# Kernel optimization log

Measured on AMD Instinct MI355X. Metric: run time of the kernel, lower is better.

The kernel has to match this reference:

```python
import jax, jax.numpy as jnp
import numpy as np

B, T, C, H = 4, 2048, 1024, 16
D = C // H  # head_dim = 64


def setup_inputs() -> dict:
    key = jax.random.key(0)
    ks = jax.random.split(key, 10)
    s = 1.0 / np.sqrt(C)
    inp = {
        "x": jax.random.normal(ks[0], (B, T, C), dtype=jnp.float32),
        "attention_mask": jnp.ones((B, T), dtype=jnp.int32),
        "Wq": jax.random.normal(ks[1], (C, C), dtype=jnp.float32) * s,
        "bq": jnp.zeros((C,), dtype=jnp.float32),
        "Wk": jax.random.normal(ks[2], (C, C), dtype=jnp.float32) * s,
        "bk": jnp.zeros((C,), dtype=jnp.float32),
        "Wv": jax.random.normal(ks[3], (C, C), dtype=jnp.float32) * s,
        "bv": jnp.zeros((C,), dtype=jnp.float32),
        "Wp": jax.random.normal(ks[4], (C, C), dtype=jnp.float32) * s,
        "bp": jnp.zeros((C,), dtype=jnp.float32),
    }
    return inp


def reference(x, attention_mask, Wq, bq, Wk, bk, Wv, bv, Wp, bp):
    # x: [B,T,C] -> q,k,v: [B,H,T,D]
    def heads(y):
        return y.reshape(B, T, H, D).transpose(0, 2, 1, 3)

    q = heads(x @ Wq + bq)
    k = heads(x @ Wk + bk)
    v = heads(x @ Wv + bv)

    scale = 1.0 / np.sqrt(D)
    att = jnp.einsum("bhqd,bhkd->bhqk", q, k) * scale  # [B,H,T,T]

    causal = jnp.tril(jnp.ones((T, T), dtype=bool))  # [T,T]
    mask = causal[None, None, :, :] & (attention_mask[:, None, None, :] != 0)
    att = jnp.where(mask, att, -jnp.inf)
    att = jax.nn.softmax(att, axis=-1)
    # dropout is identity in eval mode

    y = jnp.einsum("bhqk,bhkd->bhqd", att, v)  # [B,H,T,D]
    y = y.transpose(0, 2, 1, 3).reshape(B, T, C)
    return y @ Wp + bp
```

## Files before the change

kernel.cpp:

```cpp
#include <hip/hip_runtime.h>

#define BB 4
#define TT 2048
#define CC 1024
#define HH 16
#define DD 64

typedef unsigned short u16;
typedef unsigned int u32;
typedef __bf16 bf16;
typedef __attribute__((ext_vector_type(8))) bf16 bf16x8;
typedef __attribute__((ext_vector_type(8))) u16 u16x8;
typedef __attribute__((ext_vector_type(4))) u16 u16x4;
typedef __attribute__((ext_vector_type(4))) float f32x4;

static __device__ __forceinline__ u16 f2b(float f) {
  unsigned u = __builtin_bit_cast(unsigned, f);
  u += 0x7fffu + ((u >> 16) & 1u);
  return (u16)(u >> 16);
}
static __device__ __forceinline__ u16 bfc(float f) {
  return __builtin_bit_cast(u16, (__bf16)f);
}

__global__ void cvt_bf16_kernel(const float* __restrict__ src, u16* __restrict__ dst, int n8) {
  int i = blockIdx.x * blockDim.x + threadIdx.x;
  if (i >= n8) return;
  const float4* p4 = reinterpret_cast<const float4*>(src) + (size_t)i * 2;
  float4 a = p4[0], b = p4[1];
  u16x8 o;
  o[0] = f2b(a.x); o[1] = f2b(a.y); o[2] = f2b(a.z); o[3] = f2b(a.w);
  o[4] = f2b(b.x); o[5] = f2b(b.y); o[6] = f2b(b.z); o[7] = f2b(b.w);
  *reinterpret_cast<u16x8*>(dst + (size_t)i * 8) = o;
}

__global__ void transp_w_kernel(const float* __restrict__ w0, const float* __restrict__ w1,
                                const float* __restrict__ w2, const float* __restrict__ w3,
                                u16* __restrict__ wqkvT, u16* __restrict__ wpT) {
  __shared__ float t[32][33];
  int z = blockIdx.z;
  const float* src = z == 0 ? w0 : z == 1 ? w1 : z == 2 ? w2 : w3;
  u16* dst = z < 3 ? wqkvT + (size_t)z * CC * CC : wpT;
  int k0 = blockIdx.x * 32, n0 = blockIdx.y * 32;
  int tx = threadIdx.x & 31, ty = threadIdx.x >> 5;
#pragma unroll
  for (int i = 0; i < 4; ++i)
    t[ty + i * 8][tx] = src[(size_t)(k0 + ty + i * 8) * CC + n0 + tx];
  __syncthreads();
#pragma unroll
  for (int i = 0; i < 4; ++i)
    dst[(size_t)(n0 + ty + i * 8) * CC + k0 + tx] = f2b(t[tx][ty + i * 8]);
}

__global__ void mask_prep_kernel(const int* __restrict__ am, float* __restrict__ gm,
                                 u32* __restrict__ fwords) {
  __shared__ u32 sf[32];
  int b = blockIdx.x;
  int lane = threadIdx.x & 63, w = threadIdx.x >> 6;
#pragma unroll
  for (int j = 0; j < 8; ++j) {
    int c = w * 8 + j;
    int i = c * 64 + lane;
    int v = am[b * TT + i];
    gm[b * TT + i] = v ? 0.f : -1e30f;
    unsigned long long bal = __ballot(v != 0);
    if (lane == 0) sf[c] = (bal == ~0ull) ? 1u : 0u;
  }
  __syncthreads();
  if (threadIdx.x == 0) {
    u32 fw = 0;
    for (int c = 0; c < 32; ++c) fw |= sf[c] << c;
    fwords[b] = fw;
  }
}

__global__ __launch_bounds__(512, 2) void qkv_gemm_kernel(
    const u16* __restrict__ A, const u16* __restrict__ Bt,
    const float* __restrict__ bq, const float* __restrict__ bk, const float* __restrict__ bv,
    u16* __restrict__ q_out, u16* __restrict__ k_out, u16* __restrict__ v_out) {
  __shared__ __align__(16) char LDS[131072];
  const int tid = threadIdx.x, lane = tid & 63, w = tid >> 6;
  const int wm = w >> 2, wn = w & 3;
  const int lq = lane & 15, g = lane >> 4;
  const int m0 = blockIdx.x * 256, n0 = blockIdx.y * 256;

  const int l3 = lane >> 3;
  const int swb = ((lane & 7) ^ (l3 & 7)) * 16;
  const char* pS[8];
#pragma unroll
  for (int h = 0; h < 2; ++h)
#pragma unroll
    for (int r = 0; r < 2; ++r) {
      int row = h * 128 + r * 64 + w * 8 + l3;
      pS[h * 2 + r]     = (const char*)A  + (size_t)(m0 + row) * 2048 + swb;
      pS[4 + h * 2 + r] = (const char*)Bt + (size_t)(n0 + row) * 2048 + swb;
    }

  auto STAGE = [&](int db, int t) {
    const int off = t * 128;
#pragma unroll
    for (int m = 0; m < 2; ++m)
#pragma unroll
      for (int h = 0; h < 2; ++h)
#pragma unroll
        for (int r = 0; r < 2; ++r)
          __builtin_amdgcn_global_load_lds(
              (const __attribute__((address_space(1))) void*)(pS[m * 4 + h * 2 + r] + off),
              (__attribute__((address_space(3))) void*)(
                  LDS + m * 65536 + db * 32768 + h * 16384 + r * 8192 + w * 1024),
              16, 0, 0);
  };

  const int acol0 = (g * 16) ^ ((lq & 7) << 4);
  const int acol1 = (64 + g * 16) ^ ((lq & 7) << 4);
  const int aBase = wm * 16384 + lq * 128;
  const int bBase = 65536 + (wn >> 1) * 16384 + ((wn & 1) * 64 + lq) * 128;

  f32x4 acc[8][4] = {};

  auto TILE = [&](int db, int t) {
    if (t == 15)
      asm volatile("s_waitcnt vmcnt(0)" ::: "memory");
    else
      asm volatile("s_waitcnt vmcnt(8)" ::: "memory");
    asm volatile("s_barrier" ::: "memory");
    const char* la = LDS + db * 32768 + aBase;
    const char* lb = LDS + db * 32768 + bBase;
#pragma unroll
    for (int i4 = 0; i4 < 2; ++i4) {
      bf16x8 af[4][2];
#pragma unroll
      for (int i = 0; i < 4; ++i) {
        af[i][0] = *reinterpret_cast<const bf16x8*>(la + (i4 * 4 + i) * 2048 + acol0);
        af[i][1] = *reinterpret_cast<const bf16x8*>(la + (i4 * 4 + i) * 2048 + acol1);
      }
#pragma unroll
      for (int j2 = 0; j2 < 2; ++j2) {
        bf16x8 bfr[2][2];
#pragma unroll
        for (int j = 0; j < 2; ++j) {
          bfr[j][0] = *reinterpret_cast<const bf16x8*>(lb + (j2 * 2 + j) * 2048 + acol0);
          bfr[j][1] = *reinterpret_cast<const bf16x8*>(lb + (j2 * 2 + j) * 2048 + acol1);
        }
        __builtin_amdgcn_s_setprio(1);
#pragma unroll
        for (int i = 0; i < 4; ++i)
#pragma unroll
          for (int j = 0; j < 2; ++j) {
            f32x4& a = acc[i4 * 4 + i][j2 * 2 + j];
            a = __builtin_amdgcn_mfma_f32_16x16x32_bf16(af[i][0], bfr[j][0], a, 0, 0, 0);
            a = __builtin_amdgcn_mfma_f32_16x16x32_bf16(af[i][1], bfr[j][1], a, 0, 0, 0);
          }
        __builtin_amdgcn_s_setprio(0);
      }
    }
    asm volatile("s_barrier" ::: "memory");
    if (t + 2 < 16) STAGE(db, t + 2);
  };

  STAGE(0, 0);
  STAGE(1, 1);
  for (int t = 0; t < 16; t += 2) {
    TILE(0, t);
    TILE(1, t + 1);
  }

  const int g3 = n0 >> 10;
  const int mrow = m0 + wm * 128;
  const int ncol = n0 + wn * 64;
  if (g3 < 2) {
    u16* dst = g3 == 0 ? q_out : k_out;
    const float* bias = g3 == 0 ? bq : bk;
    const float scl = g3 == 0 ? 0.18033688f : 1.0f;
#pragma unroll
    for (int i = 0; i < 8; ++i)
#pragma unroll
      for (int j = 0; j < 4; ++j) {
        int n = ncol + j * 16 + lq;
        int h = (n >> 6) & 15, d = n & 63;
        float bb = bias[n & 1023];
#pragma unroll
        for (int r = 0; r < 4; ++r) {
          int m = mrow + i * 16 + g * 4 + r;
          int b = m >> 11, t = m & 2047;
          dst[(((size_t)(b * HH + h)) * TT + t) * DD + d] = f2b((acc[i][j][r] + bb) * scl);
        }
      }
  } else {
#pragma unroll
    for (int i = 0; i < 8; ++i)
#pragma unroll
      for (int j = 0; j < 4; ++j) {
        int n = ncol + j * 16 + lq;
        int h = (n >> 6) & 15, d = n & 63;
        float bb = bv[n & 1023];
        int mb = mrow + i * 16 + g * 4;
        int b = mb >> 11, t = mb & 2047;
        u16x4 vv;
#pragma unroll
        for (int r = 0; r < 4; ++r) vv[r] = f2b(acc[i][j][r] + bb);
        *reinterpret_cast<u16x4*>(v_out + (((size_t)(b * HH + h)) * DD + d) * TT + t) = vv;
      }
  }
}

__global__ __launch_bounds__(256) void proj_gemm_kernel(
    const u16* __restrict__ A, const u16* __restrict__ Bt,
    const float* __restrict__ bias, float* __restrict__ f_out) {
  __shared__ u16 As[2][128 * 32];
  __shared__ u16 Bs[2][128 * 32];
  const int tid = threadIdx.x, lane = tid & 63, w = tid >> 6;
  const int wm = w >> 1, wn = w & 1;
  const int m0 = blockIdx.x * 128, n0 = blockIdx.y * 128;
  const int lrow = lane >> 2, lcol = (lane & 3) * 8;
  f32x4 acc[4][4] = {};

  auto STAGE = [&](int db, int kt) {
    const int k0 = kt * 32;
#pragma unroll
    for (int r = 0; r < 2; ++r) {
      int row = r * 64 + w * 16 + lrow;
      __builtin_amdgcn_global_load_lds(
          (const __attribute__((address_space(1))) void*)(A + (size_t)(m0 + row) * CC + k0 + lcol),
          (__attribute__((address_space(3))) void*)(&As[db][(r * 64 + w * 16) * 32]), 16, 0, 0);
      __builtin_amdgcn_global_load_lds(
          (const __attribute__((address_space(1))) void*)(Bt + (size_t)(n0 + row) * CC + k0 + lcol),
          (__attribute__((address_space(3))) void*)(&Bs[db][(r * 64 + w * 16) * 32]), 16, 0, 0);
    }
  };

  STAGE(0, 0);
  STAGE(1, 1);
  for (int kt = 0; kt < 32; ++kt) {
    if (kt == 31)
      asm volatile("s_waitcnt vmcnt(0)" ::: "memory");
    else
      asm volatile("s_waitcnt vmcnt(4)" ::: "memory");
    asm volatile("s_barrier" ::: "memory");
    const int db = kt & 1;
    bf16x8 af[4], bfr[4];
#pragma unroll
    for (int i = 0; i < 4; ++i) {
      af[i] = *reinterpret_cast<const bf16x8*>(&As[db][(wm * 64 + i * 16 + (lane & 15)) * 32 + (lane >> 4) * 8]);
      bfr[i] = *reinterpret_cast<const bf16x8*>(&Bs[db][(wn * 64 + i * 16 + (lane & 15)) * 32 + (lane >> 4) * 8]);
    }
    __builtin_amdgcn_s_setprio(1);
#pragma unroll
    for (int i = 0; i < 4; ++i)
#pragma unroll
      for (int j = 0; j < 4; ++j)
        acc[i][j] = __builtin_amdgcn_mfma_f32_16x16x32_bf16(af[i], bfr[j], acc[i][j], 0, 0, 0);
    __builtin_amdgcn_s_setprio(0);
    asm volatile("s_barrier" ::: "memory");
    if (kt + 2 < 32) STAGE(db, kt + 2);
  }

  const int mrow = m0 + wm * 64;
  const int ncol = n0 + wn * 64;
#pragma unroll
  for (int i = 0; i < 4; ++i)
#pragma unroll
    for (int j = 0; j < 4; ++j)
#pragma unroll
      for (int r = 0; r < 4; ++r) {
        int m = mrow + i * 16 + (lane >> 4) * 4 + r;
        int n = ncol + j * 16 + (lane & 15);
        f_out[(size_t)m * CC + n] = acc[i][j][r] + bias[n];
      }
}

__global__ __launch_bounds__(256, 2) void attn_kernel(
    const u16* __restrict__ Q, const u16* __restrict__ K, const u16* __restrict__ Vt,
    const float* __restrict__ gm, const u32* __restrict__ fwords, u16* __restrict__ Y) {
  __shared__ __align__(16) char LDS[51200];
  const int flat = blockIdx.x;
  const int xcd = flat & 7, idx = flat >> 3;
  const int bh = xcd * 8 + (idx & 7);
  const int jb = 15 - (idx >> 3);
  const int b = bh >> 4, h = bh & 15;
  const int tid = threadIdx.x, lane = tid & 63, w = tid >> 6;
  const int lq = lane & 15, g = lane >> 4;
  const int qt = 4 * jb + w;
  const int q0 = qt * 32;
  const int nkt = (qt >> 1) + 1;
  const int nktm = 2 * jb + 2;
  const u32 fw = fwords[b];

  const u16* Qb = Q + (size_t)bh * TT * DD;
  const char* Kb = (const char*)(K + (size_t)bh * TT * DD);
  const char* Vb = (const char*)(Vt + (size_t)bh * DD * TT);

  const int l3 = lane >> 3, l7 = lane & 7;
  const int swb = (l7 * 16) ^ (l3 << 4);
  const char* kp0 = Kb + (2 * w + 0) * 1024 + l3 * 128 + swb;
  const char* kp1 = Kb + (2 * w + 1) * 1024 + l3 * 128 + swb;
  const char* vp0 = Vb + (size_t)((2 * w + 0) * 8 + l3) * 4096 + swb;
  const char* vp1 = Vb + (size_t)((2 * w + 1) * 8 + l3) * 4096 + swb;

  const int sw2 = (lq & 7) << 4;
  const int fb0 = lq * 128 + ((g * 16) ^ sw2);
  const int fb1 = lq * 128 + (((64) + g * 16) ^ sw2);
  const int pwb = 32768 + w * 4608 + lq * 144 + g * 8;
  const int prb = 32768 + w * 4608 + lq * 144 + g * 16;

  auto STAGE = [&](int buf, int kt2) {
    const int ko = kt2 * 8192, vo = kt2 * 128, lb = buf * 8192;
    __builtin_amdgcn_global_load_lds(
        (const __attribute__((address_space(1))) void*)(kp0 + ko),
        (__attribute__((address_space(3))) void*)(LDS + lb + (2 * w + 0) * 1024), 16, 0, 0);
    __builtin_amdgcn_global_load_lds(
        (const __attribute__((address_space(1))) void*)(kp1 + ko),
        (__attribute__((address_space(3))) void*)(LDS + lb + (2 * w + 1) * 1024), 16, 0, 0);
    __builtin_amdgcn_global_load_lds(
        (const __attribute__((address_space(1))) void*)(vp0 + vo),
        (__attribute__((address_space(3))) void*)(LDS + 16384 + lb + (2 * w + 0) * 1024), 16, 0, 0);
    __builtin_amdgcn_global_load_lds(
        (const __attribute__((address_space(1))) void*)(vp1 + vo),
        (__attribute__((address_space(3))) void*)(LDS + 16384 + lb + (2 * w + 1) * 1024), 16, 0, 0);
  };

  bf16x8 qf[2][2];
#pragma unroll
  for (int n = 0; n < 2; ++n)
#pragma unroll
    for (int ks = 0; ks < 2; ++ks)
      qf[n][ks] = *reinterpret_cast<const bf16x8*>(
          Qb + (size_t)(q0 + n * 16 + lq) * DD + ks * 32 + g * 8);

  f32x4 o[4][2] = {};
  float mrun[2] = {-1e30f, -1e30f};
  float lrun[2] = {0.f, 0.f};
  const f32x4 z4 = {0.f, 0.f, 0.f, 0.f};

  STAGE(0, 0);
  STAGE(1, 1);

  auto TILE = [&](int BUF, int kt) {
    if (kt < nktm - 1)
      asm volatile("s_waitcnt vmcnt(4)" ::: "memory");
    else
      asm volatile("s_waitcnt vmcnt(0)" ::: "memory");
    asm volatile("s_barrier" ::: "memory");

    if (kt < nkt) {
      const int kv0 = kt * 64;
      bf16x8 kf0[4], kf1[4];
#pragma unroll
      for (int m = 0; m < 4; ++m) {
        kf0[m] = *reinterpret_cast<const bf16x8*>(LDS + BUF * 8192 + m * 2048 + fb0);
        kf1[m] = *reinterpret_cast<const bf16x8*>(LDS + BUF * 8192 + m * 2048 + fb1);
      }
      f32x4 s[4][2];
      __builtin_amdgcn_s_setprio(1);
#pragma unroll
      for (int m = 0; m < 4; ++m)
#pragma unroll
        for (int n = 0; n < 2; ++n) {
          s[m][n] = __builtin_amdgcn_mfma_f32_16x16x32_bf16(kf0[m], qf[n][0], z4, 0, 0, 0);
          s[m][n] = __builtin_amdgcn_mfma_f32_16x16x32_bf16(kf1[m], qf[n][1], s[m][n], 0, 0, 0);
        }
      __builtin_amdgcn_s_setprio(0);

      if (!((fw >> kt) & 1u)) {
#pragma unroll
        for (int m = 0; m < 4; ++m) {
          float4 mv = *reinterpret_cast<const float4*>(gm + b * TT + kv0 + m * 16 + g * 4);
#pragma unroll
          for (int n = 0; n < 2; ++n) {
            s[m][n][0] += mv.x; s[m][n][1] += mv.y;
            s[m][n][2] += mv.z; s[m][n][3] += mv.w;
          }
        }
      }
      if (kt == nkt - 1) {
#pragma unroll
        for (int n = 0; n < 2; ++n) {
          const int q = q0 + n * 16 + lq;
#pragma unroll
          for (int m = 0; m < 4; ++m)
#pragma unroll
            for (int r = 0; r < 4; ++r) {
              int kv = kv0 + m * 16 + g * 4 + r;
              s[m][n][r] = (kv <= q) ? s[m][n][r] : -1e30f;
            }
        }
      }

#pragma unroll
      for (int n = 0; n < 2; ++n) {
        float rm = fmaxf(fmaxf(fmaxf(s[0][n][0], s[0][n][1]), fmaxf(s[0][n][2], s[0][n][3])),
                         fmaxf(fmaxf(s[1][n][0], s[1][n][1]), fmaxf(s[1][n][2], s[1][n][3])));
        float rm2 = fmaxf(fmaxf(fmaxf(s[2][n][0], s[2][n][1]), fmaxf(s[2][n][2], s[2][n][3])),
                          fmaxf(fmaxf(s[3][n][0], s[3][n][1]), fmaxf(s[3][n][2], s[3][n][3])));
        rm = fmaxf(rm, rm2);
        if (!__all(rm <= mrun[n] + 8.f)) {
          float rg = fmaxf(rm, __shfl_xor(rm, 16));
          rg = fmaxf(rg, __shfl_xor(rg, 32));
          float mnew = fmaxf(mrun[n], rg);
          float corr = __builtin_exp2f(mrun[n] - mnew);
          mrun[n] = mnew;
          lrun[n] *= corr;
#pragma unroll
          for (int nd = 0; nd < 4; ++nd)
#pragma unroll
            for (int r = 0; r < 4; ++r) o[nd][n][r] *= corr;
        }
        const float mn = mrun[n];
        float rs = 0.f;
#pragma unroll
        for (int m = 0; m < 4; ++m) {
          float p0 = __builtin_exp2f(s[m][n][0] - mn);
          float p1 = __builtin_exp2f(s[m][n][1] - mn);
          float p2 = __builtin_exp2f(s[m][n][2] - mn);
          float p3 = __builtin_exp2f(s[m][n][3] - mn);
          rs += (p0 + p1) + (p2 + p3);
          u32 wa, wb;
          asm("v_cvt_pk_bf16_f32 %0, %1, %2" : "=v"(wa) : "v"(p0), "v"(p1));
          asm("v_cvt_pk_bf16_f32 %0, %1, %2" : "=v"(wb) : "v"(p2), "v"(p3));
          uint2 pw; pw.x = wa; pw.y = wb;
          *reinterpret_cast<uint2*>(LDS + pwb + n * 2304 + m * 32) = pw;
        }
        lrun[n] += rs;
      }

      asm volatile("s_waitcnt lgkmcnt(0)" ::: "memory");
      __builtin_amdgcn_sched_barrier(0);

      __builtin_amdgcn_s_setprio(1);
#pragma unroll
      for (int ks = 0; ks < 2; ++ks) {
        const int fb = ks ? fb1 : fb0;
        bf16x8 pf0 = *reinterpret_cast<const bf16x8*>(LDS + prb + 0 * 2304 + ks * 64);
        bf16x8 pf1 = *reinterpret_cast<const bf16x8*>(LDS + prb + 1 * 2304 + ks * 64);
#pragma unroll
        for (int nd = 0; nd < 4; ++nd) {
          bf16x8 vf = *reinterpret_cast<const bf16x8*>(LDS + 16384 + BUF * 8192 + nd * 2048 + fb);
          o[nd][0] = __builtin_amdgcn_mfma_f32_16x16x32_bf16(vf, pf0, o[nd][0], 0, 0, 0);
          o[nd][1] = __builtin_amdgcn_mfma_f32_16x16x32_bf16(vf, pf1, o[nd][1], 0, 0, 0);
        }
      }
      __builtin_amdgcn_s_setprio(0);
    }

    asm volatile("s_barrier" ::: "memory");
    if (kt + 2 < nktm) STAGE(BUF, kt + 2);
  };

  for (int kt = 0; kt < nktm; kt += 2) {
    TILE(0, kt);
    TILE(1, kt + 1);
  }

#pragma unroll
  for (int n = 0; n < 2; ++n) {
    float l = lrun[n];
    l += __shfl_xor(l, 16);
    l += __shfl_xor(l, 32);
    float inv = 1.0f / l;
    const int q = q0 + n * 16 + lq;
#pragma unroll
    for (int nd = 0; nd < 4; ++nd) {
      u16x4 yv;
#pragma unroll
      for (int r = 0; r < 4; ++r) yv[r] = bfc(o[nd][n][r] * inv);
      *reinterpret_cast<u16x4*>(
          Y + ((size_t)(b * TT + q)) * CC + h * DD + nd * 16 + g * 4) = yv;
    }
  }
}

extern "C" void kernel_launch(void* const* d_in, const int* in_sizes, int n_in,
                              void* d_out, int out_size, void* d_ws, size_t ws_size,
                              hipStream_t stream) {
  const float* x  = (const float*)d_in[0];
  const int*   am = (const int*)d_in[1];
  const float* Wq = (const float*)d_in[2];
  const float* bq = (const float*)d_in[3];
  const float* Wk = (const float*)d_in[4];
  const float* bk = (const float*)d_in[5];
  const float* Wv = (const float*)d_in[6];
  const float* bv = (const float*)d_in[7];
  const float* Wp = (const float*)d_in[8];
  const float* bp = (const float*)d_in[9];
  float* out = (float*)d_out;

  char* ws = (char*)d_ws;
  u16* xb    = (u16*)(ws);
  u16* wqkvT = (u16*)(ws + (16ull << 20));
  u16* wpT   = (u16*)(ws + (22ull << 20));
  u16* qw    = (u16*)(ws + (24ull << 20));
  u16* kw    = (u16*)(ws + (40ull << 20));
  u16* vw    = (u16*)(ws + (56ull << 20));
  u16* yb    = (u16*)(ws + (72ull << 20));
  float* gm  = (float*)d_out;
  u32* fwords = (u32*)((char*)d_out + (64ull << 10));

  mask_prep_kernel<<<dim3(BB), 256, 0, stream>>>(am, gm, fwords);
  {
    int n8 = BB * TT * CC / 8;
    cvt_bf16_kernel<<<n8 / 256, 256, 0, stream>>>(x, xb, n8);
  }
  transp_w_kernel<<<dim3(32, 32, 4), 256, 0, stream>>>(Wq, Wk, Wv, Wp, wqkvT, wpT);
  qkv_gemm_kernel<<<dim3(32, 12), 512, 0, stream>>>(
      xb, wqkvT, bq, bk, bv, qw, kw, vw);
  attn_kernel<<<dim3(1024), 256, 0, stream>>>(qw, kw, vw, gm, fwords, yb);
  proj_gemm_kernel<<<dim3(64, 8), 256, 0, stream>>>(yb, wpT, bp, out);
}
```

Measured before the change: 186.2 us.

## Merge prep kernels into one launch and compute softmax row sums via MFMA

Merges the three preprocessing kernels (x conversion, weight transpose, mask prep) into a single launch that dispatches on block index, removing two kernel launches and their gaps. In attention, the per-lane running row sum is replaced by an extra MFMA against a ones vector on the same bf16 P fragments, which drops the VALU adds and the final cross-lane shuffles. The row max uses v_max3 to cut instruction count. The MFMA sum now accumulates bf16-rounded probabilities, so the normaliser differs slightly from the fp32 sum, and two extra MFMAs are issued per k-step.

```diff
diff --git a/kernel.cpp b/kernel.cpp
--- a/kernel.cpp
+++ b/kernel.cpp
@@ -22,55 +22,61 @@
 static __device__ __forceinline__ u16 bfc(float f) {
   return __builtin_bit_cast(u16, (__bf16)f);
 }
-
-__global__ void cvt_bf16_kernel(const float* __restrict__ src, u16* __restrict__ dst, int n8) {
-  int i = blockIdx.x * blockDim.x + threadIdx.x;
-  if (i >= n8) return;
-  const float4* p4 = reinterpret_cast<const float4*>(src) + (size_t)i * 2;
-  float4 a = p4[0], b = p4[1];
-  u16x8 o;
-  o[0] = f2b(a.x); o[1] = f2b(a.y); o[2] = f2b(a.z); o[3] = f2b(a.w);
-  o[4] = f2b(b.x); o[5] = f2b(b.y); o[6] = f2b(b.z); o[7] = f2b(b.w);
-  *reinterpret_cast<u16x8*>(dst + (size_t)i * 8) = o;
-}
-
-__global__ void transp_w_kernel(const float* __restrict__ w0, const float* __restrict__ w1,
-                                const float* __restrict__ w2, const float* __restrict__ w3,
-                                u16* __restrict__ wqkvT, u16* __restrict__ wpT) {
+static __device__ __forceinline__ float max3f(float a, float b, float c) {
+  float d;
+  asm("v_max3_f32 %0, %1, %2, %3" : "=v"(d) : "v"(a), "v"(b), "v"(c));
+  return d;
+}
+
+__global__ __launch_bounds__(256) void prep_kernel(
+    const float* __restrict__ x, const int* __restrict__ am,
+    const float* __restrict__ w0, const float* __restrict__ w1,
+    const float* __restrict__ w2, const float* __restrict__ w3,
+    u16* __restrict__ xb, u16* __restrict__ wqkvT, u16* __restrict__ wpT,
+    float* __restrict__ gm, u32* __restrict__ fwords) {
   __shared__ float t[32][33];
-  int z = blockIdx.z;
-  const float* src = z == 0 ? w0 : z == 1 ? w1 : z == 2 ? w2 : w3;
-  u16* dst = z < 3 ? wqkvT + (size_t)z * CC * CC : wpT;
-  int k0 = blockIdx.x * 32, n0 = blockIdx.y * 32;
-  int tx = threadIdx.x & 31, ty = threadIdx.x >> 5;
-#pragma unroll
-  for (int i = 0; i < 4; ++i)
-    t[ty + i * 8][tx] = src[(size_t)(k0 + ty + i * 8) * CC + n0 + tx];
-  __syncthreads();
-#pragma unroll
-  for (int i = 0; i < 4; ++i)
-    dst[(size_t)(n0 + ty + i * 8) * CC + k0 + tx] = f2b(t[tx][ty + i * 8]);
-}
-
-__global__ void mask_prep_kernel(const int* __restrict__ am, float* __restrict__ gm,
-                                 u32* __restrict__ fwords) {
-  __shared__ u32 sf[32];
-  int b = blockIdx.x;
-  int lane = threadIdx.x & 63, w = threadIdx.x >> 6;
-#pragma unroll
-  for (int j = 0; j < 8; ++j) {
-    int c = w * 8 + j;
-    int i = c * 64 + lane;
-    int v = am[b * TT + i];
-    gm[b * TT + i] = v ? 0.f : -1e30f;
-    unsigned long long bal = __ballot(v != 0);
-    if (lane == 0) sf[c] = (bal == ~0ull) ? 1u : 0u;
-  }
-  __syncthreads();
-  if (threadIdx.x == 0) {
-    u32 fw = 0;
-    for (int c = 0; c < 32; ++c) fw |= sf[c] << c;
-    fwords[b] = fw;
+  const int bid = blockIdx.x, tid = threadIdx.x;
+  if (bid < 4096) {
+    int i = bid * 256 + tid;
+    const float4* p4 = reinterpret_cast<const float4*>(x) + (size_t)i * 2;
+    float4 a = p4[0], b = p4[1];
+    u16x8 o;
+    o[0] = f2b(a.x); o[1] = f2b(a.y); o[2] = f2b(a.z); o[3] = f2b(a.w);
+    o[4] = f2b(b.x); o[5] = f2b(b.y); o[6] = f2b(b.z); o[7] = f2b(b.w);
+    *reinterpret_cast<u16x8*>(xb + (size_t)i * 8) = o;
+  } else if (bid < 8192) {
+    int r2 = bid - 4096;
+    int z = r2 >> 10, rem = r2 & 1023;
+    int k0 = (rem & 31) * 32, n0 = (rem >> 5) * 32;
+    const float* src = z == 0 ? w0 : z == 1 ? w1 : z == 2 ? w2 : w3;
+    u16* dst = z < 3 ? wqkvT + (size_t)z * CC * CC : wpT;
+    int tx = tid & 31, ty = tid >> 5;
+#pragma unroll
+    for (int i = 0; i < 4; ++i)
+      t[ty + i * 8][tx] = src[(size_t)(k0 + ty + i * 8) * CC + n0 + tx];
+    __syncthreads();
+#pragma unroll
+    for (int i = 0; i < 4; ++i)
+      dst[(size_t)(n0 + ty + i * 8) * CC + k0 + tx] = f2b(t[tx][ty + i * 8]);
+  } else {
+    __shared__ u32 sf[32];
+    int b = bid - 8192;
+    int lane = tid & 63, w = tid >> 6;
+#pragma unroll
+    for (int j = 0; j < 8; ++j) {
+      int c = w * 8 + j;
+      int i = c * 64 + lane;
+      int v = am[b * TT + i];
+      gm[b * TT + i] = v ? 0.f : -1e30f;
+      unsigned long long bal = __ballot(v != 0);
+      if (lane == 0) sf[c] = (bal == ~0ull) ? 1u : 0u;
+    }
+    __syncthreads();
+    if (tid == 0) {
+      u32 fw = 0;
+      for (int c = 0; c < 32; ++c) fw |= sf[c] << c;
+      fwords[b] = fw;
+    }
   }
 }
 
@@ -327,9 +333,12 @@
       qf[n][ks] = *reinterpret_cast<const bf16x8*>(
           Qb + (size_t)(q0 + n * 16 + lq) * DD + ks * 32 + g * 8);
 
+  const u16x8 onesu = {0x3F80, 0x3F80, 0x3F80, 0x3F80, 0x3F80, 0x3F80, 0x3F80, 0x3F80};
+  const bf16x8 ones = __builtin_bit_cast(bf16x8, onesu);
+
   f32x4 o[4][2] = {};
+  f32x4 l_acc[2] = {};
   float mrun[2] = {-1e30f, -1e30f};
-  float lrun[2] = {0.f, 0.f};
   const f32x4 z4 = {0.f, 0.f, 0.f, 0.f};
 
   STAGE(0, 0);
@@ -388,39 +397,37 @@
 
 #pragma unroll
       for (int n = 0; n < 2; ++n) {
-        float rm = fmaxf(fmaxf(fmaxf(s[0][n][0], s[0][n][1]), fmaxf(s[0][n][2], s[0][n][3])),
-                         fmaxf(fmaxf(s[1][n][0], s[1][n][1]), fmaxf(s[1][n][2], s[1][n][3])));
-        float rm2 = fmaxf(fmaxf(fmaxf(s[2][n][0], s[2][n][1]), fmaxf(s[2][n][2], s[2][n][3])),
-                          fmaxf(fmaxf(s[3][n][0], s[3][n][1]), fmaxf(s[3][n][2], s[3][n][3])));
-        rm = fmaxf(rm, rm2);
+        float m1 = max3f(s[0][n][0], s[0][n][1], s[0][n][2]);
+        float m2 = max3f(s[0][n][3], s[1][n][0], s[1][n][1]);
+        float m3 = max3f(s[1][n][2], s[1][n][3], s[2][n][0]);
+        float m4 = max3f(s[2][n][1], s[2][n][2], s[2][n][3]);
+        float m5 = max3f(s[3][n][0], s[3][n][1], s[3][n][2]);
+        float rm = fmaxf(max3f(m1, m2, m3), max3f(m4, m5, s[3][n][3]));
         if (!__all(rm <= mrun[n] + 8.f)) {
           float rg = fmaxf(rm, __shfl_xor(rm, 16));
           rg = fmaxf(rg, __shfl_xor(rg, 32));
           float mnew = fmaxf(mrun[n], rg);
           float corr = __builtin_exp2f(mrun[n] - mnew);
           mrun[n] = mnew;
-          lrun[n] *= corr;
+          l_acc[n] *= corr;
 #pragma unroll
           for (int nd = 0; nd < 4; ++nd)
 #pragma unroll
             for (int r = 0; r < 4; ++r) o[nd][n][r] *= corr;
         }
         const float mn = mrun[n];
-        float rs = 0.f;
 #pragma unroll
         for (int m = 0; m < 4; ++m) {
           float p0 = __builtin_exp2f(s[m][n][0] - mn);
           float p1 = __builtin_exp2f(s[m][n][1] - mn);
           float p2 = __builtin_exp2f(s[m][n][2] - mn);
           float p3 = __builtin_exp2f(s[m][n][3] - mn);
-          rs += (p0 + p1) + (p2 + p3);
           u32 wa, wb;
           asm("v_cvt_pk_bf16_f32 %0, %1, %2" : "=v"(wa) : "v"(p0), "v"(p1));
           asm("v_cvt_pk_bf16_f32 %0, %1, %2" : "=v"(wb) : "v"(p2), "v"(p3));
           uint2 pw; pw.x = wa; pw.y = wb;
           *reinterpret_cast<uint2*>(LDS + pwb + n * 2304 + m * 32) = pw;
         }
-        lrun[n] += rs;
       }
 
       asm volatile("s_waitcnt lgkmcnt(0)" ::: "memory");
@@ -438,6 +445,8 @@
           o[nd][0] = __builtin_amdgcn_mfma_f32_16x16x32_bf16(vf, pf0, o[nd][0], 0, 0, 0);
           o[nd][1] = __builtin_amdgcn_mfma_f32_16x16x32_bf16(vf, pf1, o[nd][1], 0, 0, 0);
         }
+        l_acc[0] = __builtin_amdgcn_mfma_f32_16x16x32_bf16(ones, pf0, l_acc[0], 0, 0, 0);
+        l_acc[1] = __builtin_amdgcn_mfma_f32_16x16x32_bf16(ones, pf1, l_acc[1], 0, 0, 0);
       }
       __builtin_amdgcn_s_setprio(0);
     }
@@ -453,10 +462,7 @@
 
 #pragma unroll
   for (int n = 0; n < 2; ++n) {
-    float l = lrun[n];
-    l += __shfl_xor(l, 16);
-    l += __shfl_xor(l, 32);
-    float inv = 1.0f / l;
+    float inv = 1.0f / l_acc[n][0];
     const int q = q0 + n * 16 + lq;
 #pragma unroll
     for (int nd = 0; nd < 4; ++nd) {
@@ -495,12 +501,8 @@
   float* gm  = (float*)d_out;
   u32* fwords = (u32*)((char*)d_out + (64ull << 10));
 
-  mask_prep_kernel<<<dim3(BB), 256, 0, stream>>>(am, gm, fwords);
-  {
-    int n8 = BB * TT * CC / 8;
-    cvt_bf16_kernel<<<n8 / 256, 256, 0, stream>>>(x, xb, n8);
-  }
-  transp_w_kernel<<<dim3(32, 32, 4), 256, 0, stream>>>(Wq, Wk, Wv, Wp, wqkvT, wpT);
+  prep_kernel<<<dim3(8196), 256, 0, stream>>>(
+      x, am, Wq, Wk, Wv, Wp, xb, wqkvT, wpT, gm, fwords);
   qkv_gemm_kernel<<<dim3(32, 12), 512, 0, stream>>>(
       xb, wqkvT, bq, bk, bv, qw, kw, vw);
   attn_kernel<<<dim3(1024), 256, 0, stream>>>(qw, kw, vw, gm, fwords, yb);
```

After: 174.0 us. -6.6%, faster.
